# Kernel optimization log

Hardware: AMD Instinct MI355X
Metric: run time of the kernel (lower is better)

## Reference

```python
import jax, jax.numpy as jnp
import numpy as np

NUM_GRAPHS = 100_000
NODES_PER_GRAPH = 38
NUM_NODES = NUM_GRAPHS * NODES_PER_GRAPH
NUM_EDGES = 60_800_000


def setup_inputs() -> dict:
    key = jax.random.key(0)
    ks = jax.random.split(key, 12)
    x = jax.random.normal(ks[0], (NUM_NODES, 1), dtype=jnp.float32)
    edge_index = jax.random.randint(ks[1], (2, NUM_EDGES), 0, NUM_NODES, dtype=jnp.int32)
    edge_attr = jax.random.normal(ks[2], (NUM_EDGES, 1), dtype=jnp.float32)
    # NNConv(1, 1, Linear(1, 1), aggr='add') params
    conv_root = jax.random.normal(ks[3], (1, 1), dtype=jnp.float32)
    conv_bias = jax.random.normal(ks[4], (1,), dtype=jnp.float32) * 0.1
    edge_nn_w = jax.random.normal(ks[5], (1, 1), dtype=jnp.float32)
    edge_nn_b = jax.random.normal(ks[6], (1,), dtype=jnp.float32) * 0.1
    # dense head params: 38 -> 4 -> 4 -> 1
    W1 = jax.random.normal(ks[7], (38, 4), dtype=jnp.float32) * (1.0 / np.sqrt(38))
    b1 = jax.random.normal(ks[8], (4,), dtype=jnp.float32) * 0.1
    W2 = jax.random.normal(ks[9], (4, 4), dtype=jnp.float32) * 0.5
    b2 = jax.random.normal(ks[10], (4,), dtype=jnp.float32) * 0.1
    W3 = jax.random.normal(ks[11], (4, 1), dtype=jnp.float32) * 0.5
    b3 = jnp.zeros((1,), dtype=jnp.float32)
    return {"x": x, "edge_index": edge_index, "edge_attr": edge_attr,
            "conv_root": conv_root, "conv_bias": conv_bias,
            "edge_nn_w": edge_nn_w, "edge_nn_b": edge_nn_b,
            "W1": W1, "b1": b1, "W2": W2, "b2": b2, "W3": W3, "b3": b3}


def reference(x, edge_index, edge_attr, conv_root, conv_bias,
              edge_nn_w, edge_nn_b, W1, b1, W2, b2, W3, b3):
    src, dst = edge_index[0], edge_index[1]  # messages flow src -> dst
    # edge-conditioned weight: Linear(1,1) on edge_attr -> [E,1] (in*out = 1)
    w_e = edge_attr @ edge_nn_w + edge_nn_b            # [E, 1]
    msg = x[src] * w_e                                  # gather + per-edge scale, [E, 1]
    agg = jax.ops.segment_sum(msg, dst, num_segments=NUM_NODES)  # scatter-add, [N, 1]
    nodes = x @ conv_root + agg + conv_bias             # [N, 1]
    h = nodes.reshape(NUM_GRAPHS, NODES_PER_GRAPH)      # [G, 38]
    h = jax.nn.relu(h @ W1 + b1)
    h = jax.nn.relu(h @ W2 + b2)
    out = jax.nn.sigmoid(h @ W3 + b3) * 11.0            # [G, 1]
    return out
```

## Files before the change

kernel.cpp:

```cpp
#include <hip/hip_runtime.h>
#include <hip/hip_fp16.h>
#include <math.h>

constexpr int NG  = 100000;
constexpr int NPG = 38;
constexpr int NN  = NG * NPG;
constexpr long long NE = 60800000LL;

constexpr int BIN_SHIFT = 14;
constexpr int BINW      = 1 << BIN_SHIFT;
constexpr int NB        = (NN + BINW - 1) / BINW;

constexpr int NR    = 4;
constexpr int I4_R  = (int)(NE / 4 / NR);
constexpr int NBLK1 = 1000;
constexpr int I4_B  = I4_R / NBLK1;
constexpr int CHUNK = 4096;
constexpr int CH_I4 = CHUNK / 4;

constexpr int CAPS1 = 68096;
constexpr int CAPD  = 267264;
constexpr int NB2   = 4;
constexpr int NSPLIT = 2;

constexpr size_t AGG_BYTES  = (size_t)NN * 4;
constexpr size_t XH_OFF     = AGG_BYTES;
constexpr size_t XH_BYTES   = (size_t)NB * BINW * 2;
constexpr size_t CUR1_OFF   = XH_OFF + XH_BYTES;
constexpr size_t CUR2_OFF   = CUR1_OFF + 1024;
constexpr size_t PSTRIDE    = (size_t)NB * BINW;
constexpr size_t PART_OFF   = ((CUR2_OFF + 1024 + 255) / 256) * 256;
constexpr size_t PART_BYTES = (size_t)NSPLIT * PSTRIDE * 4;
constexpr size_t REG1_OFF   = PART_OFF + PART_BYTES;
constexpr size_t REG1_BYTES = (size_t)NB * CAPS1 * 8;
constexpr size_t REG2_OFF   = REG1_OFF + REG1_BYTES;
constexpr size_t REG2_BYTES = (size_t)NB * CAPD * 4;
constexpr size_t WS_NEEDED  = REG2_OFF + REG2_BYTES;

__global__ void __launch_bounds__(256) xcast_kernel(
    const float* __restrict__ x, __half2* __restrict__ xh2)
{
    const int i = blockIdx.x * 256 + threadIdx.x;
    if (i < NN / 4) {
        float4 v = ((const float4*)x)[i];
        xh2[2 * i + 0] = __floats2half2_rn(v.x, v.y);
        xh2[2 * i + 1] = __floats2half2_rn(v.z, v.w);
    }
}

__global__ void __launch_bounds__(512) p1_kernel(
    const int*   __restrict__ ei,
    const float* __restrict__ ea,
    const float* __restrict__ wptr,
    const float* __restrict__ bptr,
    unsigned long long* __restrict__ reg1,
    int* __restrict__ cur1,
    int roff)
{
    __shared__ unsigned long long sbuf[CHUNK];
    __shared__ unsigned char     sbin[CHUNK];
    __shared__ int s_scan[256];
    __shared__ int gofs[NB];

    const int t = threadIdx.x;
    if (t < 256) s_scan[t] = 0;
    __syncthreads();

    const float w = wptr[0], b = bptr[0];
    const int4*   src4 = (const int4*)ei + roff + (size_t)blockIdx.x * I4_B;
    const int4*   dst4 = (const int4*)(ei + NE) + roff + (size_t)blockIdx.x * I4_B;
    const float4* ea4  = (const float4*)ea + roff + (size_t)blockIdx.x * I4_B;

    for (int c0 = 0; c0 < I4_B; c0 += CH_I4) {
        const int n4 = min(CH_I4, I4_B - c0);
        int rbin[8]; unsigned long long rpk[8]; int rpos[8];
        #pragma unroll
        for (int u = 0; u < 2; ++u) {
            const int j = u * 512 + t;
            const bool act = j < n4;
            int4   s4 = act ? src4[c0 + j] : make_int4(0, 0, 0, 0);
            int4   d4 = act ? dst4[c0 + j] : make_int4(0, 0, 0, 0);
            float4 e4 = act ? ea4[c0 + j]  : make_float4(0.f, 0.f, 0.f, 0.f);
            int   ss[4] = {s4.x, s4.y, s4.z, s4.w};
            int   dd[4] = {d4.x, d4.y, d4.z, d4.w};
            float ee[4] = {e4.x, e4.y, e4.z, e4.w};
            #pragma unroll
            for (int k = 0; k < 4; ++k) {
                const int idx = u * 4 + k;
                if (act) {
                    const int bin = ss[k] >> BIN_SHIFT;
                    __half_raw hr = __float2half_rn(ee[k] * w + b);
                    rbin[idx] = bin;
                    rpk[idx]  = ((unsigned long long)(unsigned)(ss[k] & (BINW - 1)) << 38)
                              | ((unsigned long long)(unsigned)dd[k] << 16)
                              | (unsigned long long)(unsigned short)hr.x;
                    rpos[idx] = atomicAdd(&s_scan[bin], 1);
                } else { rbin[idx] = -1; rpk[idx] = 0; rpos[idx] = 0; }
            }
        }
        __syncthreads();

        int acc = 0;
        if (t < 256) acc = s_scan[t];
        for (int off = 1; off < 256; off <<= 1) {
            int tmp = 0;
            if (t < 256 && t >= off) tmp = s_scan[t - off];
            __syncthreads();
            if (t < 256) { acc += tmp; s_scan[t] = acc; }
            __syncthreads();
        }

        if (t < NB) {
            const int excl = (t == 0) ? 0 : s_scan[t - 1];
            const int rl   = s_scan[t] - excl;
            gofs[t] = (rl > 0) ? atomicAdd(&cur1[t], rl) : 0;
        }
        #pragma unroll
        for (int k = 0; k < 8; ++k) {
            if (rbin[k] >= 0) {
                const int excl = (rbin[k] == 0) ? 0 : s_scan[rbin[k] - 1];
                const int idx  = excl + rpos[k];
                sbuf[idx] = rpk[k];
                sbin[idx] = (unsigned char)rbin[k];
            }
        }
        __syncthreads();

        const int tot = n4 * 4;
        for (int k = t; k < tot; k += 512) {
            const unsigned long long r = sbuf[k];
            const int bin  = sbin[k];
            const int excl = (bin == 0) ? 0 : s_scan[bin - 1];
            reg1[(size_t)bin * CAPS1 + gofs[bin] + (k - excl)] = r;
        }
        __syncthreads();
        if (t < 256) s_scan[t] = 0;
        __syncthreads();
    }
}

__global__ void __launch_bounds__(512) p2_kernel(
    const __half* __restrict__ xh,
    const unsigned long long* __restrict__ reg1,
    const int* __restrict__ cur1,
    unsigned int* __restrict__ reg2,
    int* __restrict__ cur2)
{
    __shared__ __half        xsl[BINW];
    __shared__ unsigned int  sbuf[CHUNK];
    __shared__ unsigned char sbin[CHUNK];
    __shared__ int s_scan[256];
    __shared__ int gofs[NB];

    const int t  = threadIdx.x;
    const int sb = blockIdx.x >> 2;
    const int jb = blockIdx.x & 3;

    {
        const uint4* s = (const uint4*)(xh + (size_t)sb * BINW);
        uint4* d = (uint4*)xsl;
        for (int i = t; i < BINW / 8; i += 512) d[i] = s[i];
    }
    if (t < 256) s_scan[t] = 0;
    __syncthreads();

    const int n2    = cur1[sb];
    const int cpb   = (n2 + NB2 - 1) / NB2;
    const int start = jb * cpb;
    const int end   = min(start + cpb, n2);
    const unsigned long long* seg = reg1 + (size_t)sb * CAPS1;

    for (int c0 = start; c0 < end; c0 += CHUNK) {
        const int cnt = min(CHUNK, end - c0);
        int rbin[8]; unsigned int rpk[8]; int rpos[8];
        #pragma unroll
        for (int u = 0; u < 8; ++u) {
            const int j = u * 512 + t;
            if (j < cnt) {
                const unsigned long long r = seg[c0 + j];
                const int srclow        = (int)(r >> 38);
                const unsigned int dst  = (unsigned int)(r >> 16) & 0x3FFFFFu;
                __half_raw hm; hm.x = (unsigned short)(r & 0xFFFFu);
                const float msg = __half2float(xsl[srclow]) * __half2float(__half(hm));
                __half_raw ho = __float2half_rn(msg);
                const int bin = (int)(dst >> BIN_SHIFT);
                rbin[u] = bin;
                rpk[u]  = ((dst & (unsigned)(BINW - 1)) << 16) | (unsigned int)(unsigned short)ho.x;
                rpos[u] = atomicAdd(&s_scan[bin], 1);
            } else { rbin[u] = -1; rpk[u] = 0; rpos[u] = 0; }
        }
        __syncthreads();

        int acc = 0;
        if (t < 256) acc = s_scan[t];
        for (int off = 1; off < 256; off <<= 1) {
            int tmp = 0;
            if (t < 256 && t >= off) tmp = s_scan[t - off];
            __syncthreads();
            if (t < 256) { acc += tmp; s_scan[t] = acc; }
            __syncthreads();
        }

        if (t < NB) {
            const int excl = (t == 0) ? 0 : s_scan[t - 1];
            const int rl   = s_scan[t] - excl;
            gofs[t] = (rl > 0) ? atomicAdd(&cur2[t], rl) : 0;
        }
        #pragma unroll
        for (int u = 0; u < 8; ++u) {
            if (rbin[u] >= 0) {
                const int excl = (rbin[u] == 0) ? 0 : s_scan[rbin[u] - 1];
                const int idx  = excl + rpos[u];
                sbuf[idx] = rpk[u];
                sbin[idx] = (unsigned char)rbin[u];
            }
        }
        __syncthreads();

        for (int k = t; k < cnt; k += 512) {
            const unsigned int r = sbuf[k];
            const int bin  = sbin[k];
            const int excl = (bin == 0) ? 0 : s_scan[bin - 1];
            reg2[(size_t)bin * CAPD + gofs[bin] + (k - excl)] = r;
        }
        __syncthreads();
        if (t < 256) s_scan[t] = 0;
        __syncthreads();
    }
}

__global__ void __launch_bounds__(1024) reduce_kernel(
    const unsigned int* __restrict__ reg2,
    const int* __restrict__ cur2,
    float* __restrict__ part_agg)
{
    __shared__ float acc[BINW];
    const int t    = threadIdx.x;
    const int b    = blockIdx.x >> 1;
    const int part = blockIdx.x & 1;
    for (int i = t; i < BINW; i += 1024) acc[i] = 0.0f;
    __syncthreads();

    const int n    = cur2[b];
    const int half = n >> 1;
    const int i0   = part ? half : 0;
    const int i1   = part ? n : half;
    const unsigned int* seg = reg2 + (size_t)b * CAPD;

    unsigned int a[8], nb[8];
    int k = i0 + t;
    if (k + 7168 < i1) {
        #pragma unroll
        for (int u = 0; u < 8; ++u) a[u] = seg[k + u * 1024];
        k += 8192;
        for (; k + 7168 < i1; k += 8192) {
            #pragma unroll
            for (int u = 0; u < 8; ++u) nb[u] = seg[k + u * 1024];
            #pragma unroll
            for (int u = 0; u < 8; ++u) {
                __half_raw h; h.x = (unsigned short)(a[u] & 0xFFFFu);
                atomicAdd(&acc[a[u] >> 16], __half2float(__half(h)));
            }
            #pragma unroll
            for (int u = 0; u < 8; ++u) a[u] = nb[u];
        }
        #pragma unroll
        for (int u = 0; u < 8; ++u) {
            __half_raw h; h.x = (unsigned short)(a[u] & 0xFFFFu);
            atomicAdd(&acc[a[u] >> 16], __half2float(__half(h)));
        }
    }
    for (; k < i1; k += 1024) {
        unsigned int r = seg[k];
        __half_raw h; h.x = (unsigned short)(r & 0xFFFFu);
        atomicAdd(&acc[r >> 16], __half2float(__half(h)));
    }
    __syncthreads();

    float* dst = part_agg + (size_t)part * PSTRIDE + ((size_t)b << BIN_SHIFT);
    for (int i = t; i < BINW; i += 1024) dst[i] = acc[i];
}

__global__ void __launch_bounds__(256) edge_kernel(
    const float* __restrict__ x,
    const int*   __restrict__ ei,
    const float* __restrict__ ea,
    const float* __restrict__ wptr,
    const float* __restrict__ bptr,
    float*       __restrict__ agg)
{
    const float w = wptr[0];
    const float b = bptr[0];
    const int nvec = (int)(NE / 4);
    const int4*   src4 = (const int4*)ei;
    const int4*   dst4 = (const int4*)(ei + NE);
    const float4* ea4  = (const float4*)ea;
    const int stride = gridDim.x * blockDim.x;
    for (int i = blockIdx.x * blockDim.x + threadIdx.x; i < nvec; i += stride) {
        int4   s = src4[i];
        int4   d = dst4[i];
        float4 e = ea4[i];
        atomicAdd(&agg[d.x], x[s.x] * (e.x * w + b));
        atomicAdd(&agg[d.y], x[s.y] * (e.y * w + b));
        atomicAdd(&agg[d.z], x[s.z] * (e.z * w + b));
        atomicAdd(&agg[d.w], x[s.w] * (e.w * w + b));
    }
}

__global__ void __launch_bounds__(256) head_kernel2(
    const float* __restrict__ x,
    const float* __restrict__ p0,
    const float* __restrict__ p1,
    const float* __restrict__ conv_root,
    const float* __restrict__ conv_bias,
    const float* __restrict__ W1, const float* __restrict__ b1,
    const float* __restrict__ W2, const float* __restrict__ b2,
    const float* __restrict__ W3, const float* __restrict__ b3,
    float* __restrict__ out)
{
    __shared__ float nv[256 * NPG];
    const float cr = conv_root[0];
    const float cb = conv_bias[0];

    const int gbase = blockIdx.x * 256;
    const int gcount = (NG - gbase < 256) ? (NG - gbase) : 256;
    const int fcount = gcount * NPG;
    const long long nbase = (long long)gbase * NPG;

    for (int k = threadIdx.x; k < fcount; k += 256) {
        long long gi = nbase + k;
        nv[k] = x[gi] * cr + p0[gi] + p1[gi] + cb;
    }
    __syncthreads();

    const int g = gbase + threadIdx.x;
    if (g < NG) {
        const float* p = &nv[threadIdx.x * NPG];
        float h0 = b1[0], h1 = b1[1], h2 = b1[2], h3 = b1[3];
        #pragma unroll
        for (int j = 0; j < NPG; ++j) {
            float v = p[j];
            h0 += v * W1[j * 4 + 0];
            h1 += v * W1[j * 4 + 1];
            h2 += v * W1[j * 4 + 2];
            h3 += v * W1[j * 4 + 3];
        }
        h0 = fmaxf(h0, 0.f); h1 = fmaxf(h1, 0.f);
        h2 = fmaxf(h2, 0.f); h3 = fmaxf(h3, 0.f);

        float q0 = b2[0] + h0 * W2[0] + h1 * W2[4] + h2 * W2[8]  + h3 * W2[12];
        float q1 = b2[1] + h0 * W2[1] + h1 * W2[5] + h2 * W2[9]  + h3 * W2[13];
        float q2 = b2[2] + h0 * W2[2] + h1 * W2[6] + h2 * W2[10] + h3 * W2[14];
        float q3 = b2[3] + h0 * W2[3] + h1 * W2[7] + h2 * W2[11] + h3 * W2[15];
        q0 = fmaxf(q0, 0.f); q1 = fmaxf(q1, 0.f);
        q2 = fmaxf(q2, 0.f); q3 = fmaxf(q3, 0.f);

        float z = b3[0] + q0 * W3[0] + q1 * W3[1] + q2 * W3[2] + q3 * W3[3];
        float sgm = 1.0f / (1.0f + __expf(-z));
        out[g] = 11.0f * sgm;
    }
}

__global__ void __launch_bounds__(256) head_kernel(
    const float* __restrict__ x,
    const float* __restrict__ agg,
    const float* __restrict__ conv_root,
    const float* __restrict__ conv_bias,
    const float* __restrict__ W1, const float* __restrict__ b1,
    const float* __restrict__ W2, const float* __restrict__ b2,
    const float* __restrict__ W3, const float* __restrict__ b3,
    float* __restrict__ out)
{
    __shared__ float nv[256 * NPG];
    const float cr = conv_root[0];
    const float cb = conv_bias[0];

    const int gbase = blockIdx.x * 256;
    const int gcount = (NG - gbase < 256) ? (NG - gbase) : 256;
    const int fcount = gcount * NPG;
    const long long nbase = (long long)gbase * NPG;

    for (int k = threadIdx.x; k < fcount; k += 256) {
        long long gi = nbase + k;
        nv[k] = x[gi] * cr + agg[gi] + cb;
    }
    __syncthreads();

    const int g = gbase + threadIdx.x;
    if (g < NG) {
        const float* p = &nv[threadIdx.x * NPG];
        float h0 = b1[0], h1 = b1[1], h2 = b1[2], h3 = b1[3];
        #pragma unroll
        for (int j = 0; j < NPG; ++j) {
            float v = p[j];
            h0 += v * W1[j * 4 + 0];
            h1 += v * W1[j * 4 + 1];
            h2 += v * W1[j * 4 + 2];
            h3 += v * W1[j * 4 + 3];
        }
        h0 = fmaxf(h0, 0.f); h1 = fmaxf(h1, 0.f);
        h2 = fmaxf(h2, 0.f); h3 = fmaxf(h3, 0.f);

        float q0 = b2[0] + h0 * W2[0] + h1 * W2[4] + h2 * W2[8]  + h3 * W2[12];
        float q1 = b2[1] + h0 * W2[1] + h1 * W2[5] + h2 * W2[9]  + h3 * W2[13];
        float q2 = b2[2] + h0 * W2[2] + h1 * W2[6] + h2 * W2[10] + h3 * W2[14];
        float q3 = b2[3] + h0 * W2[3] + h1 * W2[7] + h2 * W2[11] + h3 * W2[15];
        q0 = fmaxf(q0, 0.f); q1 = fmaxf(q1, 0.f);
        q2 = fmaxf(q2, 0.f); q3 = fmaxf(q3, 0.f);

        float z = b3[0] + q0 * W3[0] + q1 * W3[1] + q2 * W3[2] + q3 * W3[3];
        float sgm = 1.0f / (1.0f + __expf(-z));
        out[g] = 11.0f * sgm;
    }
}

extern "C" void kernel_launch(void* const* d_in, const int* in_sizes, int n_in,
                              void* d_out, int out_size, void* d_ws, size_t ws_size,
                              hipStream_t stream) {
    const float* x         = (const float*)d_in[0];
    const int*   ei        = (const int*)  d_in[1];
    const float* ea        = (const float*)d_in[2];
    const float* conv_root = (const float*)d_in[3];
    const float* conv_bias = (const float*)d_in[4];
    const float* ew        = (const float*)d_in[5];
    const float* eb        = (const float*)d_in[6];
    const float* W1        = (const float*)d_in[7];
    const float* b1        = (const float*)d_in[8];
    const float* W2        = (const float*)d_in[9];
    const float* b2        = (const float*)d_in[10];
    const float* W3        = (const float*)d_in[11];
    const float* b3        = (const float*)d_in[12];

    char*  ws  = (char*)d_ws;
    float* agg = (float*)ws;
    float* out = (float*)d_out;

    if (ws_size >= WS_NEEDED) {
        __half*             xh    = (__half*)(ws + XH_OFF);
        int*                cur1  = (int*)(ws + CUR1_OFF);
        int*                cur2  = (int*)(ws + CUR2_OFF);
        float*              partp = (float*)(ws + PART_OFF);
        unsigned long long* reg1  = (unsigned long long*)(ws + REG1_OFF);
        unsigned int*       reg2  = (unsigned int*)(ws + REG2_OFF);

        xcast_kernel<<<(NN / 4 + 255) / 256, 256, 0, stream>>>(x, (__half2*)xh);
        hipMemsetAsync(cur2, 0, NB * sizeof(int), stream);
        for (int r = 0; r < NR; ++r) {
            hipMemsetAsync(cur1, 0, NB * sizeof(int), stream);
            p1_kernel<<<NBLK1, 512, 0, stream>>>(ei, ea, ew, eb, reg1, cur1, r * I4_R);
            p2_kernel<<<NB * NB2, 512, 0, stream>>>(xh, reg1, cur1, reg2, cur2);
        }
        reduce_kernel<<<NB * NSPLIT, 1024, 0, stream>>>(reg2, cur2, partp);

        const int hblocks = (NG + 255) / 256;
        head_kernel2<<<hblocks, 256, 0, stream>>>(x, partp, partp + PSTRIDE,
                                                  conv_root, conv_bias,
                                                  W1, b1, W2, b2, W3, b3, out);
    } else {
        hipMemsetAsync(agg, 0, AGG_BYTES, stream);
        edge_kernel<<<2048, 256, 0, stream>>>(x, ei, ea, ew, eb, agg);
        const int hblocks = (NG + 255) / 256;
        head_kernel<<<hblocks, 256, 0, stream>>>(x, agg, conv_root, conv_bias,
                                                 W1, b1, W2, b2, W3, b3, out);
    }
}
```

Baseline: 1.213 ms.

## Replace shared-memory atomic binning with wave ballot multisplit ranking

Both partition passes now rank each element inside its bin with a wavefront ballot multisplit over the 8 bin bits, writing into per-wave histograms, instead of issuing a shared-memory atomicAdd per element. A per-bin pass over the 8 wave histograms turns them into exclusive offsets before the existing block scan. This is meant to remove contended LDS atomics on hot bins. In exchange it adds 8 ballots per element, with inactive lanes routed to a dummy bin 255, plus extra LDS traffic for the histograms.

Measured after the change: 1.272 ms. +4.8%, slower.

```diff
diff --git a/kernel.cpp b/kernel.cpp
--- a/kernel.cpp
+++ b/kernel.cpp
@@ -17,6 +17,7 @@
 constexpr int I4_B  = I4_R / NBLK1;
 constexpr int CHUNK = 4096;
 constexpr int CH_I4 = CHUNK / 4;
+constexpr int NW    = 8;
 
 constexpr int CAPS1 = 68096;
 constexpr int CAPD  = 267264;
@@ -37,6 +38,23 @@
 constexpr size_t REG2_BYTES = (size_t)NB * CAPD * 4;
 constexpr size_t WS_NEEDED  = REG2_OFF + REG2_BYTES;
 
+__device__ __forceinline__ int multisplit_rank(int bin, int lane,
+                                               volatile int* whrow)
+{
+    unsigned long long m = ~0ULL;
+    #pragma unroll
+    for (int bit = 0; bit < 8; ++bit) {
+        const int bv = (bin >> bit) & 1;
+        const unsigned long long bb = __ballot(bv != 0);
+        m &= bv ? bb : ~bb;
+    }
+    const unsigned long long lower = (1ULL << lane) - 1ULL;
+    const int lr  = __popcll(m & lower);
+    const int cur = whrow[bin];
+    if (lr == 0) whrow[bin] = cur + __popcll(m);
+    return cur + lr;
+}
+
 __global__ void __launch_bounds__(256) xcast_kernel(
     const float* __restrict__ x, __half2* __restrict__ xh2)
 {
@@ -59,11 +77,16 @@
 {
     __shared__ unsigned long long sbuf[CHUNK];
     __shared__ unsigned char     sbin[CHUNK];
+    __shared__ int whist[NW][256];
     __shared__ int s_scan[256];
     __shared__ int gofs[NB];
 
-    const int t = threadIdx.x;
-    if (t < 256) s_scan[t] = 0;
+    const int t    = threadIdx.x;
+    const int lane = t & 63;
+    const int wv   = t >> 6;
+    volatile int* whrow = &whist[wv][0];
+
+    for (int i = lane; i < 256; i += 64) whist[wv][i] = 0;
     __syncthreads();
 
     const float w = wptr[0], b = bptr[0];
@@ -73,30 +96,44 @@
 
     for (int c0 = 0; c0 < I4_B; c0 += CH_I4) {
         const int n4 = min(CH_I4, I4_B - c0);
-        int rbin[8]; unsigned long long rpk[8]; int rpos[8];
+        int rbin[8]; unsigned long long rpk[8]; int rrank[8];
         #pragma unroll
         for (int u = 0; u < 2; ++u) {
             const int j = u * 512 + t;
             const bool act = j < n4;
-            int4   s4 = act ? src4[c0 + j] : make_int4(0, 0, 0, 0);
-            int4   d4 = act ? dst4[c0 + j] : make_int4(0, 0, 0, 0);
-            float4 e4 = act ? ea4[c0 + j]  : make_float4(0.f, 0.f, 0.f, 0.f);
+            int4   s4 = make_int4(0, 0, 0, 0);
+            int4   d4 = make_int4(0, 0, 0, 0);
+            float4 e4 = make_float4(0.f, 0.f, 0.f, 0.f);
+            if (act) { s4 = src4[c0 + j]; d4 = dst4[c0 + j]; e4 = ea4[c0 + j]; }
             int   ss[4] = {s4.x, s4.y, s4.z, s4.w};
             int   dd[4] = {d4.x, d4.y, d4.z, d4.w};
             float ee[4] = {e4.x, e4.y, e4.z, e4.w};
             #pragma unroll
             for (int k = 0; k < 4; ++k) {
                 const int idx = u * 4 + k;
+                int bin = 255;
+                unsigned long long pk = 0;
                 if (act) {
-                    const int bin = ss[k] >> BIN_SHIFT;
+                    bin = ss[k] >> BIN_SHIFT;
                     __half_raw hr = __float2half_rn(ee[k] * w + b);
-                    rbin[idx] = bin;
-                    rpk[idx]  = ((unsigned long long)(unsigned)(ss[k] & (BINW - 1)) << 38)
-                              | ((unsigned long long)(unsigned)dd[k] << 16)
-                              | (unsigned long long)(unsigned short)hr.x;
-                    rpos[idx] = atomicAdd(&s_scan[bin], 1);
-                } else { rbin[idx] = -1; rpk[idx] = 0; rpos[idx] = 0; }
-            }
+                    pk = ((unsigned long long)(unsigned)(ss[k] & (BINW - 1)) << 38)
+                       | ((unsigned long long)(unsigned)dd[k] << 16)
+                       | (unsigned long long)(unsigned short)hr.x;
+                }
+                rbin[idx]  = bin;
+                rpk[idx]   = pk;
+                rrank[idx] = multisplit_rank(bin, lane, whrow);
+            }
+        }
+        __syncthreads();
+
+        if (t < 256) {
+            int s = 0;
+            #pragma unroll
+            for (int wv2 = 0; wv2 < NW; ++wv2) {
+                int c = whist[wv2][t]; whist[wv2][t] = s; s += c;
+            }
+            s_scan[t] = s;
         }
         __syncthreads();
 
@@ -117,16 +154,16 @@
         }
         #pragma unroll
         for (int k = 0; k < 8; ++k) {
-            if (rbin[k] >= 0) {
+            if (rbin[k] < NB) {
                 const int excl = (rbin[k] == 0) ? 0 : s_scan[rbin[k] - 1];
-                const int idx  = excl + rpos[k];
+                const int idx  = excl + whist[wv][rbin[k]] + rrank[k];
                 sbuf[idx] = rpk[k];
                 sbin[idx] = (unsigned char)rbin[k];
             }
         }
         __syncthreads();
 
-        const int tot = n4 * 4;
+        const int tot = s_scan[NB - 1];
         for (int k = t; k < tot; k += 512) {
             const unsigned long long r = sbuf[k];
             const int bin  = sbin[k];
@@ -134,8 +171,8 @@
             reg1[(size_t)bin * CAPS1 + gofs[bin] + (k - excl)] = r;
         }
         __syncthreads();
-        if (t < 256) s_scan[t] = 0;
-        __syncthreads();
+
+        for (int i = lane; i < 256; i += 64) whist[wv][i] = 0;
     }
 }
 
@@ -149,10 +186,14 @@
     __shared__ __half        xsl[BINW];
     __shared__ unsigned int  sbuf[CHUNK];
     __shared__ unsigned char sbin[CHUNK];
+    __shared__ int whist[NW][256];
     __shared__ int s_scan[256];
     __shared__ int gofs[NB];
 
-    const int t  = threadIdx.x;
+    const int t    = threadIdx.x;
+    const int lane = t & 63;
+    const int wv   = t >> 6;
+    volatile int* whrow = &whist[wv][0];
     const int sb = blockIdx.x >> 2;
     const int jb = blockIdx.x & 3;
 
@@ -161,7 +202,7 @@
         uint4* d = (uint4*)xsl;
         for (int i = t; i < BINW / 8; i += 512) d[i] = s[i];
     }
-    if (t < 256) s_scan[t] = 0;
+    for (int i = lane; i < 256; i += 64) whist[wv][i] = 0;
     __syncthreads();
 
     const int n2    = cur1[sb];
@@ -172,10 +213,11 @@
 
     for (int c0 = start; c0 < end; c0 += CHUNK) {
         const int cnt = min(CHUNK, end - c0);
-        int rbin[8]; unsigned int rpk[8]; int rpos[8];
+        int rbin[8]; unsigned int rpk[8]; int rrank[8];
         #pragma unroll
         for (int u = 0; u < 8; ++u) {
             const int j = u * 512 + t;
+            int bin = 255; unsigned int pk = 0;
             if (j < cnt) {
                 const unsigned long long r = seg[c0 + j];
                 const int srclow        = (int)(r >> 38);
@@ -183,11 +225,22 @@
                 __half_raw hm; hm.x = (unsigned short)(r & 0xFFFFu);
                 const float msg = __half2float(xsl[srclow]) * __half2float(__half(hm));
                 __half_raw ho = __float2half_rn(msg);
-                const int bin = (int)(dst >> BIN_SHIFT);
-                rbin[u] = bin;
-                rpk[u]  = ((dst & (unsigned)(BINW - 1)) << 16) | (unsigned int)(unsigned short)ho.x;
-                rpos[u] = atomicAdd(&s_scan[bin], 1);
-            } else { rbin[u] = -1; rpk[u] = 0; rpos[u] = 0; }
+                bin = (int)(dst >> BIN_SHIFT);
+                pk  = ((dst & (unsigned)(BINW - 1)) << 16) | (unsigned int)(unsigned short)ho.x;
+            }
+            rbin[u]  = bin;
+            rpk[u]   = pk;
+            rrank[u] = multisplit_rank(bin, lane, whrow);
+        }
+        __syncthreads();
+
+        if (t < 256) {
+            int s = 0;
+            #pragma unroll
+            for (int wv2 = 0; wv2 < NW; ++wv2) {
+                int c = whist[wv2][t]; whist[wv2][t] = s; s += c;
+            }
+            s_scan[t] = s;
         }
         __syncthreads();
 
@@ -208,24 +261,25 @@
         }
         #pragma unroll
         for (int u = 0; u < 8; ++u) {
-            if (rbin[u] >= 0) {
+            if (rbin[u] < NB) {
                 const int excl = (rbin[u] == 0) ? 0 : s_scan[rbin[u] - 1];
-                const int idx  = excl + rpos[u];
+                const int idx  = excl + whist[wv][rbin[u]] + rrank[u];
                 sbuf[idx] = rpk[u];
                 sbin[idx] = (unsigned char)rbin[u];
             }
         }
         __syncthreads();
 
-        for (int k = t; k < cnt; k += 512) {
+        const int tot = s_scan[NB - 1];
+        for (int k = t; k < tot; k += 512) {
             const unsigned int r = sbuf[k];
             const int bin  = sbin[k];
             const int excl = (bin == 0) ? 0 : s_scan[bin - 1];
             reg2[(size_t)bin * CAPD + gofs[bin] + (k - excl)] = r;
         }
         __syncthreads();
-        if (t < 256) s_scan[t] = 0;
-        __syncthreads();
+
+        for (int i = lane; i < 256; i += 64) whist[wv][i] = 0;
     }
 }
 
```
